# Kernel optimization log

Hardware: AMD Instinct MI355X
Metric: run time of the kernel (lower is better)

The kernel has to match this reference:

```python
import jax, jax.numpy as jnp
import numpy as np

B, LT, LS = 4, 1024, 1024
D, H, HKV, HD, FF = 2048, 32, 8, 64, 8192
BASE, EPS = 10000.0, 1e-6


def _rope(x):
    # x: [B, L, H, hd]; interleaved (even/odd) RoPE with positions = arange(L)
    L, d = x.shape[1], x.shape[-1]
    inv = 1.0 / (BASE ** (jnp.arange(0, d, 2, dtype=jnp.float32) / d))
    f = jnp.arange(L, dtype=jnp.float32)[:, None] * inv[None, :]  # [L, d/2]
    cos = jnp.cos(f)[None, :, None, :]
    sin = jnp.sin(f)[None, :, None, :]
    xe, xo = x[..., 0::2], x[..., 1::2]
    # stack -> [..., d/2, 2] -> reshape interleaves back to even/odd slots
    return jnp.stack([xe * cos - xo * sin, xe * sin + xo * cos], axis=-1).reshape(x.shape)


def _rmsnorm(x, g):
    return x * jax.lax.rsqrt(jnp.mean(x * x, axis=-1, keepdims=True) + EPS) * g


def _attn(q_in, k_in, v_in, Wq, Wk, Wv, Wo, bo, keep, use_rope):
    Bq, Lq, _ = q_in.shape
    Lk = k_in.shape[1]
    Q = (q_in @ Wq).reshape(Bq, Lq, H, HD)
    K = (k_in @ Wk).reshape(Bq, Lk, HKV, HD)
    V = (v_in @ Wv).reshape(Bq, Lk, HKV, HD)
    if use_rope:
        Q = _rope(Q)
        K = _rope(K)
    g = H // HKV  # GQA head expansion: each kv head repeated g times consecutively
    K = jnp.repeat(K, g, axis=2)
    V = jnp.repeat(V, g, axis=2)
    s = jnp.einsum('bqhd,bkhd->bhqk', Q, K) / jnp.sqrt(jnp.float32(HD))
    s = jnp.where(keep, s, jnp.finfo(s.dtype).min)
    p = jax.nn.softmax(s, axis=-1)
    ctx = jnp.einsum('bhqk,bkhd->bqhd', p, V).reshape(Bq, Lq, H * HD)
    return ctx @ Wo + bo


def setup_inputs() -> dict:
    key = jax.random.key(0)
    ks = jax.random.split(key, 16)
    s = 0.02

    def rn(k, shp):
        return jax.random.normal(k, shp, jnp.float32) * s

    return dict(
        x=jax.random.normal(ks[0], (B, LT, D), jnp.float32),
        encoder_output=jax.random.normal(ks[1], (B, LS, D), jnp.float32),
        pad_mask=jnp.ones((B, 1, LT), bool),
        target_mask=jnp.tril(jnp.ones((LT, LT), bool)),
        cross_attn_pad_mask=jnp.ones((B, 1, LS), bool),
        Wq1=rn(ks[2], (D, D)), Wk1=rn(ks[3], (D, HKV * HD)), Wv1=rn(ks[4], (D, HKV * HD)),
        Wo1=rn(ks[5], (D, D)), bo1=jnp.zeros((D,), jnp.float32),
        Wq2=rn(ks[6], (D, D)), Wk2=rn(ks[7], (D, HKV * HD)), Wv2=rn(ks[8], (D, HKV * HD)),
        Wo2=rn(ks[9], (D, D)), bo2=jnp.zeros((D,), jnp.float32),
        g1=jnp.ones((D,), jnp.float32), g2=jnp.ones((D,), jnp.float32), g3=jnp.ones((D,), jnp.float32),
        w1=rn(ks[10], (D, FF)), b1=jnp.zeros((FF,), jnp.float32),
        w2=rn(ks[11], (D, FF)), b2=jnp.zeros((FF,), jnp.float32),
        w3=rn(ks[12], (FF, D)), b3=jnp.zeros((D,), jnp.float32),
    )


def reference(x, encoder_output, pad_mask, target_mask, cross_attn_pad_mask,
              Wq1, Wk1, Wv1, Wo1, bo1, Wq2, Wk2, Wv2, Wo2, bo2,
              g1, g2, g3, w1, b1, w2, b2, w3, b3):
    # merged keep masks per _merge_masks: causal [1,1,Lq,Lk] AND pad [B,1,1,Lk]
    keep_self = target_mask[None, None, :, :] & pad_mask[:, None, :, :]
    keep_cross = cross_attn_pad_mask[:, None, :, :]
    n = _rmsnorm(x, g1)
    x = x + _attn(n, n, n, Wq1, Wk1, Wv1, Wo1, bo1, keep_self, True)
    n = _rmsnorm(x, g2)
    x = x + _attn(n, encoder_output, encoder_output, Wq2, Wk2, Wv2, Wo2, bo2, keep_cross, False)
    n = _rmsnorm(x, g3)
    x = x + (jax.nn.silu(n @ w1 + b1) * (n @ w2 + b2)) @ w3 + b3
    return x
```

## Files before the change

kernel.cpp:

```cpp
#include <hip/hip_runtime.h>
#include <stdint.h>

#define BB 4
#define LSEQ 1024
#define DMODEL 2048
#define NH 32
#define NKV 8
#define HD 64
#define FFDIM 8192

typedef unsigned short ushort_t;
typedef __attribute__((ext_vector_type(8))) short bf16x8;
typedef __attribute__((ext_vector_type(4))) float f32x4;
typedef __attribute__((ext_vector_type(16))) float f32x16;
typedef __attribute__((ext_vector_type(8))) unsigned short ushort8;

__device__ __forceinline__ ushort_t f2bf(float f) {
  union { float f; unsigned u; } x; x.f = f;
  unsigned u = x.u;
  u += 0x7fffu + ((u >> 16) & 1u);
  return (ushort_t)(u >> 16);
}
__device__ __forceinline__ float bf2f(ushort_t h) {
  union { unsigned u; float f; } x; x.u = ((unsigned)h) << 16;
  return x.f;
}

typedef __attribute__((address_space(3))) unsigned char lds_u8_t;
typedef __attribute__((address_space(1))) const unsigned char glob_u8_t;
__device__ __forceinline__ void gload_lds16(const void* g, void* lds) {
  __builtin_amdgcn_global_load_lds((glob_u8_t*)g, (lds_u8_t*)lds, 16, 0, 0);
}

__global__ void conv_bf16_kernel(const float* __restrict__ in,
                                 ushort_t* __restrict__ out, int nchunks) {
  int i = blockIdx.x * 256 + threadIdx.x;
  if (i >= nchunks) return;
  float4 a = ((const float4*)in)[i * 2 + 0];
  float4 b = ((const float4*)in)[i * 2 + 1];
  ushort8 o;
  o[0]=f2bf(a.x); o[1]=f2bf(a.y); o[2]=f2bf(a.z); o[3]=f2bf(a.w);
  o[4]=f2bf(b.x); o[5]=f2bf(b.y); o[6]=f2bf(b.z); o[7]=f2bf(b.w);
  ((ushort8*)out)[i] = o;
}

__global__ void convT_kernel(const float* __restrict__ W, ushort_t* __restrict__ Wt,
                             int K, int N) {
  __shared__ float tile[64][65];
  const int k0 = blockIdx.y * 64, n0 = blockIdx.x * 64;
  const int t = threadIdx.x;
  const int r = t >> 2, c0 = (t & 3) * 16;
#pragma unroll
  for (int j = 0; j < 4; ++j) {
    float4 v = *(const float4*)&W[(size_t)(k0 + r) * N + n0 + c0 + j * 4];
    tile[r][c0 + j*4 + 0] = v.x; tile[r][c0 + j*4 + 1] = v.y;
    tile[r][c0 + j*4 + 2] = v.z; tile[r][c0 + j*4 + 3] = v.w;
  }
  __syncthreads();
#pragma unroll
  for (int it = 0; it < 2; ++it) {
    int ci = t + it * 256;
    int n = ci >> 3, kc = (ci & 7) * 8;
    ushort8 o;
#pragma unroll
    for (int j = 0; j < 8; ++j) o[j] = f2bf(tile[kc + j][n]);
    *(ushort8*)&Wt[(size_t)(n0 + n) * K + k0 + kc] = o;
  }
}

__global__ void rmsnorm_kernel(const float* __restrict__ x, const float* __restrict__ g,
                               ushort_t* __restrict__ out) {
  const int row = blockIdx.x, t = threadIdx.x;
  const float* xr = x + (size_t)row * DMODEL;
  float4 a = ((const float4*)xr)[t * 2 + 0];
  float4 b = ((const float4*)xr)[t * 2 + 1];
  float ssq = a.x*a.x + a.y*a.y + a.z*a.z + a.w*a.w
            + b.x*b.x + b.y*b.y + b.z*b.z + b.w*b.w;
#pragma unroll
  for (int d = 1; d < 64; d <<= 1) ssq += __shfl_xor(ssq, d);
  __shared__ float wsum[4];
  if ((t & 63) == 0) wsum[t >> 6] = ssq;
  __syncthreads();
  float tot = wsum[0] + wsum[1] + wsum[2] + wsum[3];
  float scale = rsqrtf(tot * (1.f / DMODEL) + 1e-6f);
  float4 ga = ((const float4*)g)[t * 2 + 0];
  float4 gb = ((const float4*)g)[t * 2 + 1];
  ushort8 o;
  o[0]=f2bf(a.x*scale*ga.x); o[1]=f2bf(a.y*scale*ga.y);
  o[2]=f2bf(a.z*scale*ga.z); o[3]=f2bf(a.w*scale*ga.w);
  o[4]=f2bf(b.x*scale*gb.x); o[5]=f2bf(b.y*scale*gb.y);
  o[6]=f2bf(b.z*scale*gb.z); o[7]=f2bf(b.w*scale*gb.w);
  ((ushort8*)(out + (size_t)row * DMODEL))[t] = o;
}

__global__ void rope_fill_kernel(float2* __restrict__ tab) {
  int i = blockIdx.x * 256 + threadIdx.x;
  if (i >= LSEQ * 32) return;
  int d2 = i & 31, l = i >> 5;
  float inv = expf(-((2.f * d2) / 64.f) * logf(10000.f));
  float f = (float)l * inv;
  tab[i] = make_float2(cosf(f), sinf(f));
}

__global__ void rope_apply_kernel(ushort_t* __restrict__ X, const float2* __restrict__ tab,
                                  int L, int nh, int nchunks) {
  int i = blockIdx.x * 256 + threadIdx.x;
  if (i >= nchunks) return;
  int c = i & 7;
  int tmp = i >> 3;
  int h = tmp % nh; tmp /= nh;
  int l = tmp % L;  tmp /= L;
  int b = tmp;
  ushort_t* p = X + (((size_t)(b * L + l) * nh + h) * HD) + c * 8;
  ushort8 v = *(ushort8*)p;
#pragma unroll
  for (int j = 0; j < 4; ++j) {
    int d2 = c * 4 + j;
    float2 cs = tab[l * 32 + d2];
    float e = bf2f(v[2*j]), o = bf2f(v[2*j+1]);
    v[2*j]   = f2bf(e * cs.x - o * cs.y);
    v[2*j+1] = f2bf(e * cs.y + o * cs.x);
  }
  *(ushort8*)p = v;
}

__global__ __launch_bounds__(256, 2) void gemm_bt(
    const ushort_t* __restrict__ A, const ushort_t* __restrict__ Bt,
    int M, int N, int K, int mode,
    const float* __restrict__ bias, const float* __restrict__ res,
    const ushort_t* __restrict__ aux, void* __restrict__ outp, int LkVT)
{
  __shared__ __align__(16) ushort_t As[128 * 64];
  __shared__ __align__(16) ushort_t Bs[128 * 64];
  const int tid = threadIdx.x;
  const int lane = tid & 63;
  const int wv = tid >> 6;
  const int wm = wv >> 1, wn = wv & 1;

  const int gx = gridDim.x, gy = gridDim.y;
  const int orig = blockIdx.y * gx + blockIdx.x;
  int m0, n0;
  if ((gx & 7) == 0) {
    const int xcd = orig & 7;
    const int loc = orig >> 3;
    const int cpx = gx >> 3;
    const int nl = loc / gy;
    const int ml = loc - nl * gy;
    n0 = (xcd * cpx + nl) * 128;
    m0 = ml * 128;
  } else {
    const int nwg = gx * gy;
    int swz = ((nwg & 7) == 0) ? ((orig & 7) * (nwg >> 3) + (orig >> 3)) : orig;
    m0 = (swz / gx) * 128;
    n0 = (swz % gx) * 128;
  }

  const int l31 = lane & 31, l5 = lane >> 5;
  const int ar = lane >> 3;
  const int ac = ((lane & 7) ^ ar) * 8;

  f32x16 acc[2][2];
#pragma unroll
  for (int i = 0; i < 2; ++i)
#pragma unroll
    for (int c = 0; c < 2; ++c)
#pragma unroll
      for (int r = 0; r < 16; ++r) acc[i][c][r] = 0.f;

  for (int k0 = 0; k0 < K; k0 += 64) {
#pragma unroll
    for (int it = 0; it < 4; ++it) {
      int cb = wv * 4 + it;
      int row = cb * 8 + ar;
      gload_lds16(A  + (size_t)(m0 + row) * K + k0 + ac, (void*)(As + cb * 512));
      gload_lds16(Bt + (size_t)(n0 + row) * K + k0 + ac, (void*)(Bs + cb * 512));
    }
    __syncthreads();
#pragma unroll
    for (int ks = 0; ks < 4; ++ks) {
      bf16x8 af[2], bfr[2];
#pragma unroll
      for (int mi = 0; mi < 2; ++mi) {
        const int row = wm * 64 + mi * 32 + l31;
        const int slot = ((ks * 2 + l5) ^ (row & 7));
        af[mi] = *(const bf16x8*)&As[row * 64 + slot * 8];
      }
#pragma unroll
      for (int ni = 0; ni < 2; ++ni) {
        const int row = wn * 64 + ni * 32 + l31;
        const int slot = ((ks * 2 + l5) ^ (row & 7));
        bfr[ni] = *(const bf16x8*)&Bs[row * 64 + slot * 8];
      }
#pragma unroll
      for (int mi = 0; mi < 2; ++mi)
#pragma unroll
        for (int ni = 0; ni < 2; ++ni)
          acc[mi][ni] = __builtin_amdgcn_mfma_f32_32x32x16_bf16(
              af[mi], bfr[ni], acc[mi][ni], 0, 0, 0);
    }
    __syncthreads();
  }

#pragma unroll
  for (int mi = 0; mi < 2; ++mi) {
#pragma unroll
    for (int ni = 0; ni < 2; ++ni) {
      const int col = n0 + wn * 64 + ni * 32 + l31;
      const float bv = bias ? bias[col] : 0.f;
      const int rb = m0 + wm * 64 + mi * 32 + 4 * l5;
      if (mode == 0) {
        ushort_t* ob = (ushort_t*)outp;
#pragma unroll
        for (int r = 0; r < 16; ++r)
          ob[(size_t)(rb + (r & 3) + 8 * (r >> 2)) * N + col] = f2bf(acc[mi][ni][r] + bv);
      } else if (mode == 1) {
        ushort_t* ob = (ushort_t*)outp;
#pragma unroll
        for (int r = 0; r < 16; ++r) {
          float t = acc[mi][ni][r] + bv;
          ob[(size_t)(rb + (r & 3) + 8 * (r >> 2)) * N + col] = f2bf(t / (1.f + __expf(-t)));
        }
      } else if (mode == 2) {
        ushort_t* ob = (ushort_t*)outp;
#pragma unroll
        for (int r = 0; r < 16; ++r) {
          size_t idx = (size_t)(rb + (r & 3) + 8 * (r >> 2)) * N + col;
          ob[idx] = f2bf((acc[mi][ni][r] + bv) * bf2f(aux[idx]));
        }
      } else if (mode == 3) {
        float* of = (float*)outp;
#pragma unroll
        for (int r = 0; r < 16; ++r) {
          size_t idx = (size_t)(rb + (r & 3) + 8 * (r >> 2)) * N + col;
          of[idx] = acc[mi][ni][r] + bv + res[idx];
        }
      } else {
        ushort_t* ob = (ushort_t*)outp;
        const int kvh = col >> 6, hd = col & 63;
#pragma unroll
        for (int r = 0; r < 16; ++r) {
          int row = rb + (r & 3) + 8 * (r >> 2);
          int b = row / LkVT, l = row - b * LkVT;
          ob[((size_t)((b * NKV + kvh) * HD + hd)) * LkVT + l] = f2bf(acc[mi][ni][r]);
        }
      }
    }
  }
}

template <bool CAUSAL>
__global__ __launch_bounds__(256) void attn_kernel(
    const ushort_t* __restrict__ Q, const ushort_t* __restrict__ Kb,
    const ushort_t* __restrict__ VT, ushort_t* __restrict__ ctx,
    int Lq, int Lk)
{
  __shared__ __align__(16) ushort_t Ks[64 * 72];
  __shared__ __align__(16) ushort_t Vs[64 * 72];
  __shared__ __align__(16) ushort_t Ps[4][16 * 72];

  const int tid = threadIdx.x;
  const int lane = tid & 63;
  const int w = tid >> 6;
  const int nqt = Lq >> 6;
  int bid = blockIdx.x;
  const int qt = bid % nqt; bid /= nqt;
  const int h = bid % NH;
  const int b = bid / NH;
  const int kv = h >> 2;
  const int q0 = qt * 64;
  const int l15 = lane & 15, l4 = lane >> 4;

  const ushort_t* qbase = Q + ((size_t)(b * Lq + q0 + w * 16 + l15) * NH + h) * HD;
  bf16x8 qf[2];
  qf[0] = *(const bf16x8*)(qbase + l4 * 8);
  qf[1] = *(const bf16x8*)(qbase + 32 + l4 * 8);

  f32x4 o[4];
#pragma unroll
  for (int d = 0; d < 4; ++d) o[d] = f32x4{0.f, 0.f, 0.f, 0.f};
  float mrow[4] = {-1e30f, -1e30f, -1e30f, -1e30f};
  float lrow[4] = {0.f, 0.f, 0.f, 0.f};

  const int nkt = CAUSAL ? (qt + 1) : (Lk >> 6);
  for (int kt = 0; kt < nkt; ++kt) {
#pragma unroll
    for (int it = 0; it < 2; ++it) {
      int ci = tid + it * 256;
      int r = ci >> 3, ch = (ci & 7) * 8;
      uint4 dk = *(const uint4*)(Kb + ((size_t)(b * Lk + kt * 64 + r) * NKV + kv) * HD + ch);
      *(uint4*)&Ks[r * 72 + ch] = dk;
      uint4 dv = *(const uint4*)(VT + ((size_t)((b * NKV + kv) * HD + r)) * Lk + kt * 64 + ch);
      *(uint4*)&Vs[r * 72 + ch] = dv;
    }
    __syncthreads();

    f32x4 s[4];
#pragma unroll
    for (int cb = 0; cb < 4; ++cb) {
      f32x4 a = f32x4{0.f, 0.f, 0.f, 0.f};
      a = __builtin_amdgcn_mfma_f32_16x16x32_bf16(
            qf[0], *(const bf16x8*)&Ks[(cb * 16 + l15) * 72 + l4 * 8], a, 0, 0, 0);
      a = __builtin_amdgcn_mfma_f32_16x16x32_bf16(
            qf[1], *(const bf16x8*)&Ks[(cb * 16 + l15) * 72 + 32 + l4 * 8], a, 0, 0, 0);
      s[cb] = a;
    }
    const bool diag = CAUSAL && (kt == qt);
#pragma unroll
    for (int cb = 0; cb < 4; ++cb) {
#pragma unroll
      for (int v = 0; v < 4; ++v) {
        float sv = s[cb][v] * 0.125f;
        if (diag) {
          int kpos = kt * 64 + cb * 16 + l15;
          int qpos = q0 + w * 16 + l4 * 4 + v;
          if (kpos > qpos) sv = -1e30f;
        }
        s[cb][v] = sv;
      }
    }
    float alpha[4];
#pragma unroll
    for (int v = 0; v < 4; ++v) {
      float m2 = fmaxf(fmaxf(s[0][v], s[1][v]), fmaxf(s[2][v], s[3][v]));
#pragma unroll
      for (int d = 1; d < 16; d <<= 1) m2 = fmaxf(m2, __shfl_xor(m2, d));
      float mn = fmaxf(mrow[v], m2);
      alpha[v] = __expf(mrow[v] - mn);
      mrow[v] = mn;
    }
    float psum[4] = {0.f, 0.f, 0.f, 0.f};
#pragma unroll
    for (int cb = 0; cb < 4; ++cb) {
#pragma unroll
      for (int v = 0; v < 4; ++v) {
        float p = __expf(s[cb][v] - mrow[v]);
        psum[v] += p;
        Ps[w][(l4 * 4 + v) * 72 + cb * 16 + l15] = f2bf(p);
      }
    }
#pragma unroll
    for (int v = 0; v < 4; ++v) lrow[v] = lrow[v] * alpha[v] + psum[v];
#pragma unroll
    for (int d = 0; d < 4; ++d)
#pragma unroll
      for (int v = 0; v < 4; ++v) o[d][v] *= alpha[v];

#pragma unroll
    for (int ks = 0; ks < 2; ++ks) {
      bf16x8 pa = *(const bf16x8*)&Ps[w][l15 * 72 + ks * 32 + l4 * 8];
#pragma unroll
      for (int d = 0; d < 4; ++d) {
        bf16x8 vf = *(const bf16x8*)&Vs[(d * 16 + l15) * 72 + ks * 32 + l4 * 8];
        o[d] = __builtin_amdgcn_mfma_f32_16x16x32_bf16(pa, vf, o[d], 0, 0, 0);
      }
    }
    __syncthreads();
  }

  float inv[4];
#pragma unroll
  for (int v = 0; v < 4; ++v) {
    float L = lrow[v];
#pragma unroll
    for (int d = 1; d < 16; d <<= 1) L += __shfl_xor(L, d);
    inv[v] = 1.f / L;
  }
  ushort_t* cbase = ctx + ((size_t)(b * Lq + q0 + w * 16) * NH + h) * HD;
#pragma unroll
  for (int d = 0; d < 4; ++d)
#pragma unroll
    for (int v = 0; v < 4; ++v) {
      int qloc = l4 * 4 + v;
      cbase[(size_t)qloc * NH * HD + d * 16 + l15] = f2bf(o[d][v] * inv[v]);
    }
}

extern "C" void kernel_launch(void* const* d_in, const int* in_sizes, int n_in,
                              void* d_out, int out_size, void* d_ws, size_t ws_size,
                              hipStream_t stream) {
  const float* x    = (const float*)d_in[0];
  const float* enc  = (const float*)d_in[1];
  const float* Wq1 = (const float*)d_in[5];
  const float* Wk1 = (const float*)d_in[6];
  const float* Wv1 = (const float*)d_in[7];
  const float* Wo1 = (const float*)d_in[8];
  const float* bo1 = (const float*)d_in[9];
  const float* Wq2 = (const float*)d_in[10];
  const float* Wk2 = (const float*)d_in[11];
  const float* Wv2 = (const float*)d_in[12];
  const float* Wo2 = (const float*)d_in[13];
  const float* bo2 = (const float*)d_in[14];
  const float* g1  = (const float*)d_in[15];
  const float* g2  = (const float*)d_in[16];
  const float* g3  = (const float*)d_in[17];
  const float* w1  = (const float*)d_in[18];
  const float* b1  = (const float*)d_in[19];
  const float* w2  = (const float*)d_in[20];
  const float* b2  = (const float*)d_in[21];
  const float* w3  = (const float*)d_in[22];
  const float* b3  = (const float*)d_in[23];

  const int M = BB * LSEQ;
  uint8_t* ws = (uint8_t*)d_ws;
  size_t off = 0;
  auto alloc = [&](size_t bytes) { void* p = ws + off; off += (bytes + 255) & ~(size_t)255; return p; };
  ushort_t* n_bf   = (ushort_t*)alloc((size_t)M * DMODEL * 2);
  ushort_t* enc_bf = (ushort_t*)alloc((size_t)M * DMODEL * 2);
  ushort_t* q_bf   = (ushort_t*)alloc((size_t)M * DMODEL * 2);
  ushort_t* k_bf   = (ushort_t*)alloc((size_t)M * NKV * HD * 2);
  ushort_t* vt_bf  = (ushort_t*)alloc((size_t)M * NKV * HD * 2);
  ushort_t* ctx_bf = (ushort_t*)alloc((size_t)M * DMODEL * 2);
  ushort_t* h_bf   = (ushort_t*)alloc((size_t)M * FFDIM * 2);
  ushort_t* wt     = (ushort_t*)alloc((size_t)DMODEL * FFDIM * 2);
  float2*   tab    = (float2*)alloc((size_t)LSEQ * 32 * 8);
  (void)ws_size; (void)in_sizes; (void)n_in; (void)out_size;

  float* xf = (float*)d_out;
  hipMemcpyAsync(d_out, d_in[0], (size_t)M * DMODEL * 4, hipMemcpyDeviceToDevice, stream);

  conv_bf16_kernel<<<4096, 256, 0, stream>>>(enc, enc_bf, M * DMODEL / 8);
  rope_fill_kernel<<<128, 256, 0, stream>>>(tab);

  const int KVN = NKV * HD;
  dim3 blk(256);
  auto ggrid = [](int N, int Mm) { return dim3(N / 128, Mm / 128); };
  auto tgrid = [](int K, int N) { return dim3(N / 64, K / 64); };

  rmsnorm_kernel<<<M, 256, 0, stream>>>(xf, g1, n_bf);
  convT_kernel<<<tgrid(DMODEL, DMODEL), blk, 0, stream>>>(Wq1, wt, DMODEL, DMODEL);
  gemm_bt<<<ggrid(DMODEL, M), blk, 0, stream>>>(n_bf, wt, M, DMODEL, DMODEL, 0, nullptr, nullptr, nullptr, q_bf, 1);
  convT_kernel<<<tgrid(DMODEL, KVN), blk, 0, stream>>>(Wk1, wt, DMODEL, KVN);
  gemm_bt<<<ggrid(KVN, M), blk, 0, stream>>>(n_bf, wt, M, KVN, DMODEL, 0, nullptr, nullptr, nullptr, k_bf, 1);
  rope_apply_kernel<<<(M * NH * 8) / 256, 256, 0, stream>>>(q_bf, tab, LSEQ, NH, M * NH * 8);
  rope_apply_kernel<<<(M * NKV * 8) / 256, 256, 0, stream>>>(k_bf, tab, LSEQ, NKV, M * NKV * 8);
  convT_kernel<<<tgrid(DMODEL, KVN), blk, 0, stream>>>(Wv1, wt, DMODEL, KVN);
  gemm_bt<<<ggrid(KVN, M), blk, 0, stream>>>(n_bf, wt, M, KVN, DMODEL, 4, nullptr, nullptr, nullptr, vt_bf, LSEQ);
  attn_kernel<true><<<BB * NH * (LSEQ / 64), blk, 0, stream>>>(q_bf, k_bf, vt_bf, ctx_bf, LSEQ, LSEQ);
  convT_kernel<<<tgrid(DMODEL, DMODEL), blk, 0, stream>>>(Wo1, wt, DMODEL, DMODEL);
  gemm_bt<<<ggrid(DMODEL, M), blk, 0, stream>>>(ctx_bf, wt, M, DMODEL, DMODEL, 3, bo1, xf, nullptr, xf, 1);

  rmsnorm_kernel<<<M, 256, 0, stream>>>(xf, g2, n_bf);
  convT_kernel<<<tgrid(DMODEL, DMODEL), blk, 0, stream>>>(Wq2, wt, DMODEL, DMODEL);
  gemm_bt<<<ggrid(DMODEL, M), blk, 0, stream>>>(n_bf, wt, M, DMODEL, DMODEL, 0, nullptr, nullptr, nullptr, q_bf, 1);
  convT_kernel<<<tgrid(DMODEL, KVN), blk, 0, stream>>>(Wk2, wt, DMODEL, KVN);
  gemm_bt<<<ggrid(KVN, M), blk, 0, stream>>>(enc_bf, wt, M, KVN, DMODEL, 0, nullptr, nullptr, nullptr, k_bf, 1);
  convT_kernel<<<tgrid(DMODEL, KVN), blk, 0, stream>>>(Wv2, wt, DMODEL, KVN);
  gemm_bt<<<ggrid(KVN, M), blk, 0, stream>>>(enc_bf, wt, M, KVN, DMODEL, 4, nullptr, nullptr, nullptr, vt_bf, LSEQ);
  attn_kernel<false><<<BB * NH * (LSEQ / 64), blk, 0, stream>>>(q_bf, k_bf, vt_bf, ctx_bf, LSEQ, LSEQ);
  convT_kernel<<<tgrid(DMODEL, DMODEL), blk, 0, stream>>>(Wo2, wt, DMODEL, DMODEL);
  gemm_bt<<<ggrid(DMODEL, M), blk, 0, stream>>>(ctx_bf, wt, M, DMODEL, DMODEL, 3, bo2, xf, nullptr, xf, 1);

  rmsnorm_kernel<<<M, 256, 0, stream>>>(xf, g3, n_bf);
  convT_kernel<<<tgrid(DMODEL, FFDIM), blk, 0, stream>>>(w1, wt, DMODEL, FFDIM);
  gemm_bt<<<ggrid(FFDIM, M), blk, 0, stream>>>(n_bf, wt, M, FFDIM, DMODEL, 1, b1, nullptr, nullptr, h_bf, 1);
  convT_kernel<<<tgrid(DMODEL, FFDIM), blk, 0, stream>>>(w2, wt, DMODEL, FFDIM);
  gemm_bt<<<ggrid(FFDIM, M), blk, 0, stream>>>(n_bf, wt, M, FFDIM, DMODEL, 2, b2, nullptr, h_bf, h_bf, 1);
  convT_kernel<<<tgrid(FFDIM, DMODEL), blk, 0, stream>>>(w3, wt, FFDIM, DMODEL);
  gemm_bt<<<ggrid(DMODEL, M), blk, 0, stream>>>(h_bf, wt, M, DMODEL, FFDIM, 3, b3, xf, nullptr, xf, 1);
}
```

Measured before the change: 1.223 ms.

## Fuse FFN gate and up GEMMs into one dual-B kernel with SiLU epilogue

```diff
diff --git a/kernel.cpp b/kernel.cpp
--- a/kernel.cpp
+++ b/kernel.cpp
@@ -243,6 +243,99 @@
           int b = row / LkVT, l = row - b * LkVT;
           ob[((size_t)((b * NKV + kvh) * HD + hd)) * LkVT + l] = f2bf(acc[mi][ni][r]);
         }
+      }
+    }
+  }
+}
+
+__global__ __launch_bounds__(256, 2) void gemm_ffn12(
+    const ushort_t* __restrict__ A, const ushort_t* __restrict__ B1t,
+    const ushort_t* __restrict__ B2t, int M, int N, int K,
+    const float* __restrict__ b1, const float* __restrict__ b2,
+    ushort_t* __restrict__ outp)
+{
+  __shared__ __align__(16) ushort_t As[128 * 64];
+  __shared__ __align__(16) ushort_t B1s[128 * 64];
+  __shared__ __align__(16) ushort_t B2s[128 * 64];
+  const int tid = threadIdx.x;
+  const int lane = tid & 63;
+  const int wv = tid >> 6;
+  const int wm = wv >> 1, wn = wv & 1;
+
+  const int gx = gridDim.x, gy = gridDim.y;
+  const int orig = blockIdx.y * gx + blockIdx.x;
+  const int xcd = orig & 7;
+  const int loc = orig >> 3;
+  const int cpx = gx >> 3;
+  const int nl = loc / gy;
+  const int ml = loc - nl * gy;
+  const int n0 = (xcd * cpx + nl) * 128;
+  const int m0 = ml * 128;
+
+  const int l31 = lane & 31, l5 = lane >> 5;
+  const int ar = lane >> 3;
+  const int ac = ((lane & 7) ^ ar) * 8;
+
+  f32x16 ac1[2][2], ac2[2][2];
+#pragma unroll
+  for (int i = 0; i < 2; ++i)
+#pragma unroll
+    for (int c = 0; c < 2; ++c)
+#pragma unroll
+      for (int r = 0; r < 16; ++r) { ac1[i][c][r] = 0.f; ac2[i][c][r] = 0.f; }
+
+  for (int k0 = 0; k0 < K; k0 += 64) {
+#pragma unroll
+    for (int it = 0; it < 4; ++it) {
+      int cb = wv * 4 + it;
+      int row = cb * 8 + ar;
+      gload_lds16(A   + (size_t)(m0 + row) * K + k0 + ac, (void*)(As  + cb * 512));
+      gload_lds16(B1t + (size_t)(n0 + row) * K + k0 + ac, (void*)(B1s + cb * 512));
+      gload_lds16(B2t + (size_t)(n0 + row) * K + k0 + ac, (void*)(B2s + cb * 512));
+    }
+    __syncthreads();
+#pragma unroll
+    for (int ks = 0; ks < 4; ++ks) {
+      bf16x8 af[2], b1f[2], b2f[2];
+#pragma unroll
+      for (int mi = 0; mi < 2; ++mi) {
+        const int row = wm * 64 + mi * 32 + l31;
+        const int slot = ((ks * 2 + l5) ^ (row & 7));
+        af[mi] = *(const bf16x8*)&As[row * 64 + slot * 8];
+      }
+#pragma unroll
+      for (int ni = 0; ni < 2; ++ni) {
+        const int row = wn * 64 + ni * 32 + l31;
+        const int slot = ((ks * 2 + l5) ^ (row & 7));
+        b1f[ni] = *(const bf16x8*)&B1s[row * 64 + slot * 8];
+        b2f[ni] = *(const bf16x8*)&B2s[row * 64 + slot * 8];
+      }
+#pragma unroll
+      for (int mi = 0; mi < 2; ++mi)
+#pragma unroll
+        for (int ni = 0; ni < 2; ++ni) {
+          ac1[mi][ni] = __builtin_amdgcn_mfma_f32_32x32x16_bf16(
+              af[mi], b1f[ni], ac1[mi][ni], 0, 0, 0);
+          ac2[mi][ni] = __builtin_amdgcn_mfma_f32_32x32x16_bf16(
+              af[mi], b2f[ni], ac2[mi][ni], 0, 0, 0);
+        }
+    }
+    __syncthreads();
+  }
+
+#pragma unroll
+  for (int mi = 0; mi < 2; ++mi) {
+#pragma unroll
+    for (int ni = 0; ni < 2; ++ni) {
+      const int col = n0 + wn * 64 + ni * 32 + l31;
+      const float bv1 = b1[col], bv2 = b2[col];
+      const int rb = m0 + wm * 64 + mi * 32 + 4 * l5;
+#pragma unroll
+      for (int r = 0; r < 16; ++r) {
+        float v1 = ac1[mi][ni][r] + bv1;
+        float v2 = ac2[mi][ni][r] + bv2;
+        float h = (v1 / (1.f + __expf(-v1))) * v2;
+        outp[(size_t)(rb + (r & 3) + 8 * (r >> 2)) * N + col] = f2bf(h);
       }
     }
   }
@@ -413,10 +506,10 @@
   ushort_t* h_bf   = (ushort_t*)alloc((size_t)M * FFDIM * 2);
   ushort_t* wt     = (ushort_t*)alloc((size_t)DMODEL * FFDIM * 2);
   float2*   tab    = (float2*)alloc((size_t)LSEQ * 32 * 8);
+  ushort_t* wt2    = enc_bf;
   (void)ws_size; (void)in_sizes; (void)n_in; (void)out_size;
 
   float* xf = (float*)d_out;
-  hipMemcpyAsync(d_out, d_in[0], (size_t)M * DMODEL * 4, hipMemcpyDeviceToDevice, stream);
 
   conv_bf16_kernel<<<4096, 256, 0, stream>>>(enc, enc_bf, M * DMODEL / 8);
   rope_fill_kernel<<<128, 256, 0, stream>>>(tab);
@@ -426,7 +519,7 @@
   auto ggrid = [](int N, int Mm) { return dim3(N / 128, Mm / 128); };
   auto tgrid = [](int K, int N) { return dim3(N / 64, K / 64); };
 
-  rmsnorm_kernel<<<M, 256, 0, stream>>>(xf, g1, n_bf);
+  rmsnorm_kernel<<<M, 256, 0, stream>>>(x, g1, n_bf);
   convT_kernel<<<tgrid(DMODEL, DMODEL), blk, 0, stream>>>(Wq1, wt, DMODEL, DMODEL);
   gemm_bt<<<ggrid(DMODEL, M), blk, 0, stream>>>(n_bf, wt, M, DMODEL, DMODEL, 0, nullptr, nullptr, nullptr, q_bf, 1);
   convT_kernel<<<tgrid(DMODEL, KVN), blk, 0, stream>>>(Wk1, wt, DMODEL, KVN);
@@ -437,7 +530,7 @@
   gemm_bt<<<ggrid(KVN, M), blk, 0, stream>>>(n_bf, wt, M, KVN, DMODEL, 4, nullptr, nullptr, nullptr, vt_bf, LSEQ);
   attn_kernel<true><<<BB * NH * (LSEQ / 64), blk, 0, stream>>>(q_bf, k_bf, vt_bf, ctx_bf, LSEQ, LSEQ);
   convT_kernel<<<tgrid(DMODEL, DMODEL), blk, 0, stream>>>(Wo1, wt, DMODEL, DMODEL);
-  gemm_bt<<<ggrid(DMODEL, M), blk, 0, stream>>>(ctx_bf, wt, M, DMODEL, DMODEL, 3, bo1, xf, nullptr, xf, 1);
+  gemm_bt<<<ggrid(DMODEL, M), blk, 0, stream>>>(ctx_bf, wt, M, DMODEL, DMODEL, 3, bo1, x, nullptr, xf, 1);
 
   rmsnorm_kernel<<<M, 256, 0, stream>>>(xf, g2, n_bf);
   convT_kernel<<<tgrid(DMODEL, DMODEL), blk, 0, stream>>>(Wq2, wt, DMODEL, DMODEL);
@@ -452,9 +545,8 @@
 
   rmsnorm_kernel<<<M, 256, 0, stream>>>(xf, g3, n_bf);
   convT_kernel<<<tgrid(DMODEL, FFDIM), blk, 0, stream>>>(w1, wt, DMODEL, FFDIM);
-  gemm_bt<<<ggrid(FFDIM, M), blk, 0, stream>>>(n_bf, wt, M, FFDIM, DMODEL, 1, b1, nullptr, nullptr, h_bf, 1);
-  convT_kernel<<<tgrid(DMODEL, FFDIM), blk, 0, stream>>>(w2, wt, DMODEL, FFDIM);
-  gemm_bt<<<ggrid(FFDIM, M), blk, 0, stream>>>(n_bf, wt, M, FFDIM, DMODEL, 2, b2, nullptr, h_bf, h_bf, 1);
+  convT_kernel<<<tgrid(DMODEL, FFDIM), blk, 0, stream>>>(w2, wt2, DMODEL, FFDIM);
+  gemm_ffn12<<<ggrid(FFDIM, M), blk, 0, stream>>>(n_bf, wt, wt2, M, FFDIM, DMODEL, b1, b2, h_bf);
   convT_kernel<<<tgrid(FFDIM, DMODEL), blk, 0, stream>>>(w3, wt, FFDIM, DMODEL);
   gemm_bt<<<ggrid(DMODEL, M), blk, 0, stream>>>(h_bf, wt, M, DMODEL, FFDIM, 3, b3, xf, nullptr, xf, 1);
 }
```

Measured after the change: 1.145 ms. 1.07x faster.
